# Performance work log

Hardware: AMD Instinct MI355X
Metric: run time of the kernel (lower is better)

Reference implementation:

```python
import jax, jax.numpy as jnp
import numpy as np

MAX_NEUMANN_STEPS = 8

def _neumann_inverse(A):
    # (I + A)^{-1} for strictly lower-triangular A via Neumann series with repeated squaring.
    T = A.shape[-1]
    I = jnp.eye(T, dtype=A.dtype)
    neg_A = -A
    B_power = neg_A
    N = I + neg_A
    for _ in range(MAX_NEUMANN_STEPS - 1):
        B_power = jnp.matmul(B_power, B_power)
        N = N + jnp.matmul(B_power, N)
    return N

def setup_inputs() -> dict:
    key = jax.random.key(0)
    ks = jax.random.split(key, 6)
    B, H, T, Dk, Dv = 16, 32, 256, 128, 128
    q = jax.random.normal(ks[0], (B, H, T, Dk), dtype=jnp.float32)
    k = jax.random.normal(ks[1], (B, H, T, Dk), dtype=jnp.float32)
    k = k / jnp.linalg.norm(k, axis=-1, keepdims=True)  # keys are L2-normalized
    v = jax.random.normal(ks[2], (B, H, T, Dv), dtype=jnp.float32)
    # log-space decay gate: small negative values so exp(g) in (0,1)
    g = -0.05 * jax.random.uniform(ks[3], (B, H, T), dtype=jnp.float32)
    beta = jax.random.uniform(ks[4], (B, H, T), dtype=jnp.float32)
    S0 = jax.random.normal(ks[5], (B, H, Dk, Dv), dtype=jnp.float32)
    return {"q": q, "k": k, "v": v, "g": g, "beta": beta, "last_recurrent_state": S0}

def reference(q, k, v, g, beta, last_recurrent_state):
    S = last_recurrent_state                               # (B,H,Dk,Dv)
    g_cumsum = jnp.cumsum(g, axis=-1)                      # (B,H,T)
    KKT = jnp.matmul(k, k.swapaxes(-1, -2))                # (B,H,T,T)
    g_diff = g_cumsum[..., :, None] - g_cumsum[..., None, :]
    A_full = beta[..., None] * jnp.exp(g_diff) * KKT
    A = jnp.tril(A_full, k=-1)                             # strictly lower triangular
    T_inv = _neumann_inverse(A)                            # (I+A)^{-1}
    beta_g = (beta * jnp.exp(g_cumsum))[..., None]         # (B,H,T,1)
    W = jnp.matmul(T_inv, beta_g * k)                      # (B,H,T,Dk)
    U = jnp.matmul(T_inv, beta[..., None] * v)             # (B,H,T,Dv)
    v_new = U - jnp.matmul(W, S)                           # (B,H,T,Dv)
    inter = jnp.matmul(q, S) * jnp.exp(g_cumsum)[..., None]
    QKT = jnp.matmul(q, k.swapaxes(-1, -2))
    causal = jnp.tril(jnp.exp(g_diff), k=0)
    intra = jnp.matmul(causal * QKT, v_new)
    output = inter + intra                                 # (B,H,T,Dv)
    g_last = g_cumsum[..., -1:]                            # (B,H,1)
    S_new = S * jnp.exp(g_last)[..., None]
    g_scale = jnp.exp(g_last[..., None] - g_cumsum[..., None])  # (B,H,T,1)
    S_new = S_new + jnp.matmul(k.swapaxes(-2, -1), v_new * g_scale)
    return jnp.concatenate([output.reshape(-1), S_new.reshape(-1)], axis=0)
```

## Files before the change

### kernel.cpp

```cpp
#include <hip/hip_runtime.h>
#include <hip/hip_bf16.h>

typedef __attribute__((ext_vector_type(8))) short short8;
typedef __attribute__((ext_vector_type(4))) short short4v;
typedef __attribute__((ext_vector_type(4))) float f32x4;

#define DEVI static __device__ __forceinline__

constexpr int T_SEQ = 256, DK = 128, DV = 128, CH = 64, NCH = 4;
constexpr int NPAIR = 16 * 32;
constexpr size_t OUT_ELEMS = (size_t)NPAIR * T_SEQ * DV;

constexpr int OFF_SB   = 0;
constexpr int OFF_KC   = 32768;
constexpr int OFF_KCT  = 49152;
constexpr int OFF_KRQS = 65536;
constexpr int OFF_V    = 81920;
constexpr int OFF_B    = 98304;
constexpr int OFF_BT   = 106496;
constexpr int OFF_NT   = 114688;
constexpr int OFF_GC   = 122880;
constexpr int OFF_BETA = 123904;
constexpr int OFF_EPOS = 124928;
constexpr int OFF_ENEG = 125184;
constexpr int OFF_WS   = 125440;
constexpr int LDS_BYTES = 125472;

DEVI unsigned short f2bf(float f) {
  union { float f; unsigned u; } a; a.f = f;
  unsigned r = a.u + 0x7fffu + ((a.u >> 16) & 1u);
  return (unsigned short)(r >> 16);
}
DEVI float bf2f(unsigned short h) {
  union { unsigned u; float f; } a; a.u = ((unsigned)h) << 16;
  return a.f;
}

DEVI f32x4 mfma(short8 a, short8 b, f32x4 c) {
  return __builtin_amdgcn_mfma_f32_16x16x32_bf16(a, b, c, 0, 0, 0);
}

DEVI short8 ldf(const char* s, int stride, int row, int k0) {
  return *(const short8*)(s + row * stride + ((((row & 7) << 4)) ^ (k0 * 2)));
}
DEVI void st4(char* s, int stride, int row, int col0, f32x4 v) {
  short4v p;
  p[0] = (short)f2bf(v[0]); p[1] = (short)f2bf(v[1]);
  p[2] = (short)f2bf(v[2]); p[3] = (short)f2bf(v[3]);
  *(short4v*)(s + row * stride + (((row & 7) << 4) ^ (col0 * 2))) = p;
}
DEVI void st1(char* s, int stride, int row, int col, float f) {
  *(unsigned short*)(s + row * stride + (((row & 7) << 4) ^ (col * 2))) = f2bf(f);
}

__global__ __launch_bounds__(512, 1)
void cra_fwd(const float* __restrict__ qg_, const float* __restrict__ kg_,
             const float* __restrict__ vg_, const float* __restrict__ gg_,
             const float* __restrict__ bg_, const float* __restrict__ s0g_,
             float* __restrict__ outg_)
{
  extern __shared__ char sm[];
  const int tid = threadIdx.x;
  const int lane = tid & 63, w = tid >> 6;
  const int l15 = lane & 15, l4 = lane >> 4;
  const int pair = blockIdx.x;

  const size_t rowbase = (size_t)pair * T_SEQ;
  const float* qg = qg_ + rowbase * DK;
  const float* kg = kg_ + rowbase * DK;
  const float* vg = vg_ + rowbase * DV;
  float* outg = outg_ + rowbase * DV;
  float* soutg = outg_ + OUT_ELEMS + (size_t)pair * DK * DV;

  float* gc    = (float*)(sm + OFF_GC);
  float* bet   = (float*)(sm + OFF_BETA);
  float* eposA = (float*)(sm + OFF_EPOS);
  float* enegA = (float*)(sm + OFF_ENEG);
  float* wsum  = (float*)(sm + OFF_WS);

  f32x4 Sacc[8];
  {
    const float* Sp = s0g_ + (size_t)pair * DK * DV;
    const int dk0 = w * 16 + l4 * 4;
#pragma unroll
    for (int tn = 0; tn < 8; ++tn) {
      const int dv = tn * 16 + l15;
#pragma unroll
      for (int rr = 0; rr < 4; ++rr)
        Sacc[tn][rr] = Sp[(size_t)(dk0 + rr) * DV + dv];
    }
  }

  if (tid < 256) {
    float x = gg_[rowbase + tid];
    bet[tid] = bg_[rowbase + tid];
#pragma unroll
    for (int d = 1; d < 64; d <<= 1) {
      float y = __shfl_up(x, d, 64);
      if (lane >= d) x += y;
    }
    if (lane == 63) wsum[w] = x;
    gc[tid] = x;
  }
  __syncthreads();
  if (tid < 256) {
    float pre = 0.f;
    for (int j = 0; j < w; ++j) pre += wsum[j];
    gc[tid] += pre;
  }
  __syncthreads();

  const int r = tid >> 3, u = tid & 7;
  const f32x4 zero = {0.f, 0.f, 0.f, 0.f};
  const int tmB = (w >> 1) * 16;

#pragma unroll 1
  for (int c = 0; c < NCH; ++c) {
    const int t0 = c * CH;
    if (tid < 64) {
      const float base = (c == 0) ? 0.f : gc[t0 - 1];
      const float lc = gc[t0 + tid] - base;
      eposA[tid] = __expf(lc);
      enegA[tid] = __expf(-lc);
    }
    const float4* kp = (const float4*)(kg + (size_t)(t0 + r) * DK);
    const float4* vp = (const float4*)(vg + (size_t)(t0 + r) * DV);
    float4 kv[4], vv[4];
#pragma unroll
    for (int j = 0; j < 4; ++j) { kv[j] = kp[u + 8 * j]; vv[j] = vp[u + 8 * j]; }
    __syncthreads();

    {
      const float be = bet[t0 + r], ep = eposA[r], en = enegA[r];
      const float krs = be * ep;
#pragma unroll
      for (int j = 0; j < 4; ++j) {
        const int col0 = 4 * (u + 8 * j);
        const float kf[4] = {kv[j].x, kv[j].y, kv[j].z, kv[j].w};
        const float vf[4] = {vv[j].x, vv[j].y, vv[j].z, vv[j].w};
        short4v pr, pc;
#pragma unroll
        for (int e = 0; e < 4; ++e) {
          pr[e] = (short)f2bf(kf[e] * krs);
          pc[e] = (short)f2bf(kf[e] * en);
        }
        *(short4v*)(sm + OFF_KRQS + r * 256 + (((r & 7) << 4) ^ (col0 * 2))) = pr;
        *(short4v*)(sm + OFF_KC   + r * 256 + (((r & 7) << 4) ^ (col0 * 2))) = pc;
#pragma unroll
        for (int e = 0; e < 4; ++e) {
          const int d = col0 + e;
          *(unsigned short*)(sm + OFF_KCT + d * 128 + (((d & 7) << 4) ^ (r * 2))) = f2bf(kf[e] * en);
          *(unsigned short*)(sm + OFF_V   + d * 128 + (((d & 7) << 4) ^ (r * 2))) = f2bf(vf[e] * be);
        }
      }
      const int dk0 = w * 16 + l4 * 4;
#pragma unroll
      for (int tn = 0; tn < 8; ++tn)
        st4(sm + OFF_SB, 256, tn * 16 + l15, dk0, Sacc[tn]);
    }
    __syncthreads();

    f32x4 nreg[2];
#pragma unroll
    for (int s = 0; s < 2; ++s) {
      const int tn = (w & 1) * 2 + s;
      f32x4 acc = zero;
#pragma unroll
      for (int ks = 0; ks < 4; ++ks) {
        short8 af = ldf(sm + OFF_KRQS, 256, tmB + l15,   ks * 32 + l4 * 8);
        short8 bf = ldf(sm + OFF_KC,   256, tn * 16 + l15, ks * 32 + l4 * 8);
        acc = mfma(af, bf, acc);
      }
      const int i0 = tmB + l4 * 4, jj = tn * 16 + l15;
      f32x4 nr;
#pragma unroll
      for (int rr = 0; rr < 4; ++rr) {
        const int i = i0 + rr;
        const float Bv = (i > jj) ? -acc[rr] : 0.f;
        st1(sm + OFF_B,  128, i, jj, Bv);
        st1(sm + OFF_BT, 128, jj, i, Bv);
        nr[rr] = ((i == jj) ? 1.f : 0.f) + Bv;
      }
      nreg[s] = nr;
      st4(sm + OFF_NT, 128, jj, i0, nr);
    }

#pragma unroll
    for (int s = 0; s < 4; ++s) {
      const int tn = (w & 1) * 4 + s;
      f32x4 acc = zero;
#pragma unroll
      for (int ks = 0; ks < 4; ++ks) {
        short8 af = ldf(sm + OFF_KRQS, 256, tmB + l15,   ks * 32 + l4 * 8);
        short8 bf = ldf(sm + OFF_SB,   256, tn * 16 + l15, ks * 32 + l4 * 8);
        acc = mfma(af, bf, acc);
      }
      const int dv = tn * 16 + l15, i0 = tmB + l4 * 4;
      char* p = sm + OFF_V + dv * 128 + (((dv & 7) << 4) ^ (i0 * 2));
      short4v old = *(const short4v*)p;
      short4v nw;
#pragma unroll
      for (int rr = 0; rr < 4; ++rr)
        nw[rr] = (short)f2bf(bf2f((unsigned short)old[rr]) - acc[rr]);
      *(short4v*)p = nw;
    }
    const float4* qp = (const float4*)(qg + (size_t)(t0 + r) * DK);
    float4 qv[4];
#pragma unroll
    for (int j = 0; j < 4; ++j) qv[j] = qp[u + 8 * j];
    __syncthreads();

#pragma unroll
    for (int it = 0; it < 5; ++it) {
      f32x4 b2[2];
#pragma unroll
      for (int s = 0; s < 2; ++s) {
        const int tn = (w & 1) * 2 + s;
        f32x4 acc = zero;
#pragma unroll
        for (int ks = 0; ks < 2; ++ks) {
          short8 af = ldf(sm + OFF_B,  128, tmB + l15,   ks * 32 + l4 * 8);
          short8 bf = ldf(sm + OFF_BT, 128, tn * 16 + l15, ks * 32 + l4 * 8);
          acc = mfma(af, bf, acc);
        }
        b2[s] = acc;
      }
      __syncthreads();
#pragma unroll
      for (int s = 0; s < 2; ++s) {
        const int tn = (w & 1) * 2 + s;
        const int i0 = tmB + l4 * 4, jj = tn * 16 + l15;
#pragma unroll
        for (int rr = 0; rr < 4; ++rr) st1(sm + OFF_B, 128, i0 + rr, jj, b2[s][rr]);
        if (it < 4) st4(sm + OFF_BT, 128, jj, i0, b2[s]);
      }
      __syncthreads();
#pragma unroll
      for (int s = 0; s < 2; ++s) {
        const int tn = (w & 1) * 2 + s;
#pragma unroll
        for (int ks = 0; ks < 2; ++ks) {
          short8 af = ldf(sm + OFF_B,  128, tmB + l15,   ks * 32 + l4 * 8);
          short8 bf = ldf(sm + OFF_NT, 128, tn * 16 + l15, ks * 32 + l4 * 8);
          nreg[s] = mfma(af, bf, nreg[s]);
        }
      }
      __syncthreads();
#pragma unroll
      for (int s = 0; s < 2; ++s) {
        const int tn = (w & 1) * 2 + s;
        const int i0 = tmB + l4 * 4, jj = tn * 16 + l15;
        st4(sm + OFF_NT, 128, jj, i0, nreg[s]);
        if (it == 4) {
#pragma unroll
          for (int rr = 0; rr < 4; ++rr) st1(sm + OFF_BT, 128, i0 + rr, jj, nreg[s][rr]);
        }
      }
      __syncthreads();
    }

    f32x4 vn[4];
#pragma unroll
    for (int s = 0; s < 4; ++s) {
      const int tn = (w & 1) * 4 + s;
      f32x4 acc = zero;
#pragma unroll
      for (int ks = 0; ks < 2; ++ks) {
        short8 af = ldf(sm + OFF_BT, 128, tmB + l15,   ks * 32 + l4 * 8);
        short8 bf = ldf(sm + OFF_V,  128, tn * 16 + l15, ks * 32 + l4 * 8);
        acc = mfma(af, bf, acc);
      }
      vn[s] = acc;
    }
    __syncthreads();
#pragma unroll
    for (int s = 0; s < 4; ++s) {
      const int tn = (w & 1) * 4 + s;
      st4(sm + OFF_V, 128, tn * 16 + l15, tmB + l4 * 4, vn[s]);
    }
    {
      const float ep = eposA[r];
#pragma unroll
      for (int j = 0; j < 4; ++j) {
        const int col0 = 4 * (u + 8 * j);
        const float qf[4] = {qv[j].x, qv[j].y, qv[j].z, qv[j].w};
        short4v pq;
#pragma unroll
        for (int e = 0; e < 4; ++e) pq[e] = (short)f2bf(qf[e] * ep);
        *(short4v*)(sm + OFF_KRQS + r * 256 + (((r & 7) << 4) ^ (col0 * 2))) = pq;
      }
    }
    __syncthreads();

    f32x4 outA[4];
#pragma unroll
    for (int s = 0; s < 4; ++s) {
      const int tn = (w & 1) * 4 + s;
      f32x4 acc = zero;
#pragma unroll
      for (int ks = 0; ks < 4; ++ks) {
        short8 af = ldf(sm + OFF_KRQS, 256, tmB + l15,   ks * 32 + l4 * 8);
        short8 bf = ldf(sm + OFF_SB,   256, tn * 16 + l15, ks * 32 + l4 * 8);
        acc = mfma(af, bf, acc);
      }
      outA[s] = acc;
    }
#pragma unroll
    for (int s = 0; s < 2; ++s) {
      const int tn = (w & 1) * 2 + s;
      f32x4 acc = zero;
#pragma unroll
      for (int ks = 0; ks < 4; ++ks) {
        short8 af = ldf(sm + OFF_KRQS, 256, tmB + l15,   ks * 32 + l4 * 8);
        short8 bf = ldf(sm + OFF_KC,   256, tn * 16 + l15, ks * 32 + l4 * 8);
        acc = mfma(af, bf, acc);
      }
      const int i0 = tmB + l4 * 4, jj = tn * 16 + l15;
#pragma unroll
      for (int rr = 0; rr < 4; ++rr)
        st1(sm + OFF_B, 128, i0 + rr, jj, (jj <= i0 + rr) ? acc[rr] : 0.f);
    }
    __syncthreads();
#pragma unroll
    for (int s = 0; s < 4; ++s) {
      const int tn = (w & 1) * 4 + s;
#pragma unroll
      for (int ks = 0; ks < 2; ++ks) {
        short8 af = ldf(sm + OFF_B, 128, tmB + l15,   ks * 32 + l4 * 8);
        short8 bf = ldf(sm + OFF_V, 128, tn * 16 + l15, ks * 32 + l4 * 8);
        outA[s] = mfma(af, bf, outA[s]);
      }
    }
    {
      const float eG = eposA[CH - 1];
#pragma unroll
      for (int tn = 0; tn < 8; ++tn) {
#pragma unroll
        for (int ks = 0; ks < 2; ++ks) {
          short8 af = ldf(sm + OFF_KCT, 128, w * 16 + l15,  ks * 32 + l4 * 8);
          short8 bf = ldf(sm + OFF_V,   128, tn * 16 + l15, ks * 32 + l4 * 8);
          Sacc[tn] = mfma(af, bf, Sacc[tn]);
        }
#pragma unroll
        for (int rr = 0; rr < 4; ++rr) Sacc[tn][rr] *= eG;
      }
    }
    __syncthreads();
    {
      float* OST = (float*)(sm + OFF_KC);
#pragma unroll
      for (int s = 0; s < 4; ++s) {
        const int tn = (w & 1) * 4 + s;
        const int i0 = tmB + l4 * 4, dv = tn * 16 + l15;
#pragma unroll
        for (int rr = 0; rr < 4; ++rr) OST[(i0 + rr) * 128 + dv] = outA[s][rr];
      }
    }
    __syncthreads();
    {
      float4* og = (float4*)(outg + (size_t)t0 * DV);
      const float4* os = (const float4*)(sm + OFF_KC);
#pragma unroll
      for (int j = 0; j < 4; ++j) og[tid + 512 * j] = os[tid + 512 * j];
    }
    __syncthreads();
  }

  {
    float* SST = (float*)sm;
    const int dk0 = w * 16 + l4 * 4;
#pragma unroll
    for (int tn = 0; tn < 8; ++tn) {
      const int dv = tn * 16 + l15;
#pragma unroll
      for (int rr = 0; rr < 4; ++rr) SST[(dk0 + rr) * 128 + dv] = Sacc[tn][rr];
    }
  }
  __syncthreads();
  {
    float4* sg = (float4*)soutg;
    const float4* ss = (const float4*)sm;
#pragma unroll
    for (int j = 0; j < 8; ++j) sg[tid + 512 * j] = ss[tid + 512 * j];
  }
}

extern "C" void kernel_launch(void* const* d_in, const int* in_sizes, int n_in,
                              void* d_out, int out_size, void* d_ws, size_t ws_size,
                              hipStream_t stream) {
  (void)in_sizes; (void)n_in; (void)out_size; (void)d_ws; (void)ws_size;
  const float* q  = (const float*)d_in[0];
  const float* k  = (const float*)d_in[1];
  const float* v  = (const float*)d_in[2];
  const float* g  = (const float*)d_in[3];
  const float* b  = (const float*)d_in[4];
  const float* s0 = (const float*)d_in[5];
  hipFuncSetAttribute((const void*)cra_fwd,
                      hipFuncAttributeMaxDynamicSharedMemorySize, LDS_BYTES);
  hipLaunchKernelGGL(cra_fwd, dim3(NPAIR), dim3(512), LDS_BYTES, stream,
                     q, k, v, g, b, s0, (float*)d_out);
}
```

Baseline: 305.3 us.

## Apply Neumann inverse directly to value block via ping-pong power matrices

Instead of building the explicit inverse matrix N by repeated squaring and then multiplying it into V, the loop now updates the transformed value block X in place (X += P·X) while squaring the power matrix, with ping-pong P/PT buffers. Fewer barriers per iteration are needed. LDS swizzles widen to 16-row patterns, next-chunk k/v loads are prefetched into registers, and output and final state are written straight to global memory instead of being staged through LDS. This raises LDS use and makes the final global stores less coalesced. The bf16 rounding of X on every iteration may also change accuracy.

Result: slower. 391.0 us (+28.1%).

```diff
diff --git a/kernel.cpp b/kernel.cpp
--- a/kernel.cpp
+++ b/kernel.cpp
@@ -8,23 +8,24 @@
 #define DEVI static __device__ __forceinline__
 
 constexpr int T_SEQ = 256, DK = 128, DV = 128, CH = 64, NCH = 4;
-constexpr int NPAIR = 16 * 32;
+constexpr int NPAIR = 512;
 constexpr size_t OUT_ELEMS = (size_t)NPAIR * T_SEQ * DV;
 
 constexpr int OFF_SB   = 0;
 constexpr int OFF_KC   = 32768;
-constexpr int OFF_KCT  = 49152;
-constexpr int OFF_KRQS = 65536;
-constexpr int OFF_V    = 81920;
-constexpr int OFF_B    = 98304;
-constexpr int OFF_BT   = 106496;
-constexpr int OFF_NT   = 114688;
-constexpr int OFF_GC   = 122880;
-constexpr int OFF_BETA = 123904;
-constexpr int OFF_EPOS = 124928;
-constexpr int OFF_ENEG = 125184;
-constexpr int OFF_WS   = 125440;
-constexpr int LDS_BYTES = 125472;
+constexpr int OFF_KRQS = 49152;
+constexpr int OFF_XT   = 65536;
+constexpr int OFF_KCT  = 98304;
+constexpr int OFF_PA   = 114688;
+constexpr int OFF_PTA  = 124928;
+constexpr int OFF_PB   = 135168;
+constexpr int OFF_PTB  = 145408;
+constexpr int OFF_EPOS = 155648;
+constexpr int OFF_ENEG = 155904;
+constexpr int OFF_GC   = 156160;
+constexpr int OFF_BETA = 157184;
+constexpr int OFF_WS   = 158208;
+constexpr int LDS_BYTES = 158240;
 
 DEVI unsigned short f2bf(float f) {
   union { float f; unsigned u; } a; a.f = f;
@@ -35,22 +36,26 @@
   union { unsigned u; float f; } a; a.u = ((unsigned)h) << 16;
   return a.f;
 }
-
 DEVI f32x4 mfma(short8 a, short8 b, f32x4 c) {
   return __builtin_amdgcn_mfma_f32_16x16x32_bf16(a, b, c, 0, 0, 0);
 }
-
-DEVI short8 ldf(const char* s, int stride, int row, int k0) {
-  return *(const short8*)(s + row * stride + ((((row & 7) << 4)) ^ (k0 * 2)));
-}
-DEVI void st4(char* s, int stride, int row, int col0, f32x4 v) {
+DEVI short8 ld16(const char* s, int row, int kb) {
+  return *(const short8*)(s + row * 256 + (((row & 15) << 4) ^ kb));
+}
+DEVI void st4_16(char* s, int row, int col0, short4v p) {
+  *(short4v*)(s + row * 256 + (((row & 15) << 4) ^ (col0 * 2))) = p;
+}
+DEVI short8 ld8(const char* s, int stride, int row, int kb) {
+  return *(const short8*)(s + row * stride + (((row & 7) << 4) ^ kb));
+}
+DEVI void st4_8(char* s, int stride, int row, int col0, short4v p) {
+  *(short4v*)(s + row * stride + (((row & 7) << 4) ^ (col0 * 2))) = p;
+}
+DEVI short4v pack4(f32x4 v) {
   short4v p;
   p[0] = (short)f2bf(v[0]); p[1] = (short)f2bf(v[1]);
   p[2] = (short)f2bf(v[2]); p[3] = (short)f2bf(v[3]);
-  *(short4v*)(s + row * stride + (((row & 7) << 4) ^ (col0 * 2))) = p;
-}
-DEVI void st1(char* s, int stride, int row, int col, float f) {
-  *(unsigned short*)(s + row * stride + (((row & 7) << 4) ^ (col * 2))) = f2bf(f);
+  return p;
 }
 
 __global__ __launch_bounds__(512, 1)
@@ -63,6 +68,7 @@
   const int tid = threadIdx.x;
   const int lane = tid & 63, w = tid >> 6;
   const int l15 = lane & 15, l4 = lane >> 4;
+  const int kb0 = l4 * 16;
   const int pair = blockIdx.x;
 
   const size_t rowbase = (size_t)pair * T_SEQ;
@@ -91,6 +97,14 @@
     }
   }
 
+  const int r = tid >> 3, u = tid & 7;
+  float4 kv[4], vv[4];
+  {
+    const float4* kp = (const float4*)(kg + (size_t)r * DK);
+    const float4* vp = (const float4*)(vg + (size_t)r * DV);
+#pragma unroll
+    for (int j = 0; j < 4; ++j) { kv[j] = kp[u + 8 * j]; vv[j] = vp[u + 8 * j]; }
+  }
   if (tid < 256) {
     float x = gg_[rowbase + tid];
     bet[tid] = bg_[rowbase + tid];
@@ -110,7 +124,6 @@
   }
   __syncthreads();
 
-  const int r = tid >> 3, u = tid & 7;
   const f32x4 zero = {0.f, 0.f, 0.f, 0.f};
   const int tmB = (w >> 1) * 16;
 
@@ -123,11 +136,6 @@
       eposA[tid] = __expf(lc);
       enegA[tid] = __expf(-lc);
     }
-    const float4* kp = (const float4*)(kg + (size_t)(t0 + r) * DK);
-    const float4* vp = (const float4*)(vg + (size_t)(t0 + r) * DV);
-    float4 kv[4], vv[4];
-#pragma unroll
-    for (int j = 0; j < 4; ++j) { kv[j] = kp[u + 8 * j]; vv[j] = vp[u + 8 * j]; }
     __syncthreads();
 
     {
@@ -144,244 +152,212 @@
           pr[e] = (short)f2bf(kf[e] * krs);
           pc[e] = (short)f2bf(kf[e] * en);
         }
-        *(short4v*)(sm + OFF_KRQS + r * 256 + (((r & 7) << 4) ^ (col0 * 2))) = pr;
-        *(short4v*)(sm + OFF_KC   + r * 256 + (((r & 7) << 4) ^ (col0 * 2))) = pc;
+        st4_16(sm + OFF_KRQS, r, col0, pr);
+        st4_16(sm + OFF_KC,   r, col0, pc);
 #pragma unroll
         for (int e = 0; e < 4; ++e) {
           const int d = col0 + e;
           *(unsigned short*)(sm + OFF_KCT + d * 128 + (((d & 7) << 4) ^ (r * 2))) = f2bf(kf[e] * en);
-          *(unsigned short*)(sm + OFF_V   + d * 128 + (((d & 7) << 4) ^ (r * 2))) = f2bf(vf[e] * be);
+          *(unsigned short*)(sm + OFF_XT  + d * 256 + (((d & 15) << 4) ^ (r * 2))) = f2bf(vf[e] * be);
         }
       }
       const int dk0 = w * 16 + l4 * 4;
 #pragma unroll
       for (int tn = 0; tn < 8; ++tn)
-        st4(sm + OFF_SB, 256, tn * 16 + l15, dk0, Sacc[tn]);
+        st4_16(sm + OFF_SB, tn * 16 + l15, dk0, pack4(Sacc[tn]));
     }
     __syncthreads();
 
-    f32x4 nreg[2];
+    float4 qv[4];
+    {
+      const float4* qp = (const float4*)(qg + (size_t)(t0 + r) * DK);
+#pragma unroll
+      for (int j = 0; j < 4; ++j) qv[j] = qp[u + 8 * j];
+    }
 #pragma unroll
     for (int s = 0; s < 2; ++s) {
-      const int tn = (w & 1) * 2 + s;
-      f32x4 acc = zero;
-#pragma unroll
-      for (int ks = 0; ks < 4; ++ks) {
-        short8 af = ldf(sm + OFF_KRQS, 256, tmB + l15,   ks * 32 + l4 * 8);
-        short8 bf = ldf(sm + OFF_KC,   256, tn * 16 + l15, ks * 32 + l4 * 8);
-        acc = mfma(af, bf, acc);
-      }
-      const int i0 = tmB + l4 * 4, jj = tn * 16 + l15;
-      f32x4 nr;
+      const int nt = (w & 1) * 2 + s;
+      f32x4 acc = zero;
+#pragma unroll
+      for (int ks = 0; ks < 4; ++ks)
+        acc = mfma(ld16(sm + OFF_KRQS, tmB + l15, ks * 64 + kb0),
+                   ld16(sm + OFF_KC,   nt * 16 + l15, ks * 64 + kb0), acc);
+      const int jj = nt * 16 + l15, i0 = tmB + l4 * 4;
+      short4v p;
 #pragma unroll
       for (int rr = 0; rr < 4; ++rr) {
         const int i = i0 + rr;
-        const float Bv = (i > jj) ? -acc[rr] : 0.f;
-        st1(sm + OFF_B,  128, i, jj, Bv);
-        st1(sm + OFF_BT, 128, jj, i, Bv);
-        nr[rr] = ((i == jj) ? 1.f : 0.f) + Bv;
-      }
-      nreg[s] = nr;
-      st4(sm + OFF_NT, 128, jj, i0, nr);
-    }
-
+        p[rr] = (short)f2bf((i > jj) ? -acc[rr] : 0.f);
+      }
+      st4_8(sm + OFF_PTA, 160, jj, i0, p);
+    }
+#pragma unroll
+    for (int s = 0; s < 2; ++s) {
+      const int nt = (w & 1) * 2 + s;
+      f32x4 acc = zero;
+#pragma unroll
+      for (int ks = 0; ks < 4; ++ks)
+        acc = mfma(ld16(sm + OFF_KC,   tmB + l15, ks * 64 + kb0),
+                   ld16(sm + OFF_KRQS, nt * 16 + l15, ks * 64 + kb0), acc);
+      const int ii = nt * 16 + l15, j0 = tmB + l4 * 4;
+      short4v p;
+#pragma unroll
+      for (int rr = 0; rr < 4; ++rr) {
+        const int j = j0 + rr;
+        p[rr] = (short)f2bf((ii > j) ? -acc[rr] : 0.f);
+      }
+      st4_8(sm + OFF_PA, 160, ii, j0, p);
+    }
 #pragma unroll
     for (int s = 0; s < 4; ++s) {
-      const int tn = (w & 1) * 4 + s;
-      f32x4 acc = zero;
-#pragma unroll
-      for (int ks = 0; ks < 4; ++ks) {
-        short8 af = ldf(sm + OFF_KRQS, 256, tmB + l15,   ks * 32 + l4 * 8);
-        short8 bf = ldf(sm + OFF_SB,   256, tn * 16 + l15, ks * 32 + l4 * 8);
-        acc = mfma(af, bf, acc);
-      }
-      const int dv = tn * 16 + l15, i0 = tmB + l4 * 4;
-      char* p = sm + OFF_V + dv * 128 + (((dv & 7) << 4) ^ (i0 * 2));
-      short4v old = *(const short4v*)p;
-      short4v nw;
+      const int dvt = (w & 1) * 4 + s;
+      f32x4 acc = zero;
+#pragma unroll
+      for (int ks = 0; ks < 4; ++ks)
+        acc = mfma(ld16(sm + OFF_KRQS, tmB + l15, ks * 64 + kb0),
+                   ld16(sm + OFF_SB,   dvt * 16 + l15, ks * 64 + kb0), acc);
+      const int dv = dvt * 16 + l15, i0 = tmB + l4 * 4;
+      char* p = sm + OFF_XT + dv * 256 + (((dv & 15) << 4) ^ (i0 * 2));
+      short4v old = *(const short4v*)p, nw;
 #pragma unroll
       for (int rr = 0; rr < 4; ++rr)
         nw[rr] = (short)f2bf(bf2f((unsigned short)old[rr]) - acc[rr]);
       *(short4v*)p = nw;
     }
-    const float4* qp = (const float4*)(qg + (size_t)(t0 + r) * DK);
-    float4 qv[4];
-#pragma unroll
-    for (int j = 0; j < 4; ++j) qv[j] = qp[u + 8 * j];
+
+#pragma unroll
+    for (int it = 0; it < 6; ++it) {
+      __syncthreads();
+      const char* Pc  = (it & 1) ? sm + OFF_PB  : sm + OFF_PA;
+      const char* PTc = (it & 1) ? sm + OFF_PTB : sm + OFF_PTA;
+      char* Pn  = (it & 1) ? sm + OFF_PA  : sm + OFF_PB;
+      char* PTn = (it & 1) ? sm + OFF_PTA : sm + OFF_PTB;
+
+      short8 bb[2];
+#pragma unroll
+      for (int ks = 0; ks < 2; ++ks)
+        bb[ks] = ld16(sm + OFF_XT, w * 16 + l15, ks * 64 + kb0);
+      f32x4 xa[4];
+#pragma unroll
+      for (int itile = 0; itile < 4; ++itile) {
+        f32x4 acc = zero;
+#pragma unroll
+        for (int ks = 0; ks < 2; ++ks)
+          acc = mfma(ld8(Pc, 160, itile * 16 + l15, ks * 64 + kb0), bb[ks], acc);
+        xa[itile] = acc;
+      }
+      if (it == 0) {
+        const float ep = eposA[r];
+#pragma unroll
+        for (int j = 0; j < 4; ++j) {
+          const int col0 = 4 * (u + 8 * j);
+          const float qf[4] = {qv[j].x, qv[j].y, qv[j].z, qv[j].w};
+          short4v pq;
+#pragma unroll
+          for (int e = 0; e < 4; ++e) pq[e] = (short)f2bf(qf[e] * ep);
+          st4_16(sm + OFF_KRQS, r, col0, pq);
+        }
+      }
+      if (it < 5) {
+#pragma unroll
+        for (int s = 0; s < 2; ++s) {
+          const int nt = (w & 1) * 2 + s;
+          f32x4 a1 = zero, a2 = zero;
+#pragma unroll
+          for (int ks = 0; ks < 2; ++ks) {
+            a1 = mfma(ld8(Pc,  160, tmB + l15, ks * 64 + kb0),
+                      ld8(PTc, 160, nt * 16 + l15, ks * 64 + kb0), a1);
+            a2 = mfma(ld8(PTc, 160, tmB + l15, ks * 64 + kb0),
+                      ld8(Pc,  160, nt * 16 + l15, ks * 64 + kb0), a2);
+          }
+          st4_8(PTn, 160, nt * 16 + l15, tmB + l4 * 4, pack4(a1));
+          st4_8(Pn,  160, nt * 16 + l15, tmB + l4 * 4, pack4(a2));
+        }
+      }
+#pragma unroll
+      for (int itile = 0; itile < 4; ++itile) {
+        const int row = w * 16 + l15;
+        char* p = sm + OFF_XT + row * 256 + (((row & 15) << 4) ^ ((itile * 16 + l4 * 4) * 2));
+        short4v old = *(const short4v*)p, nw;
+#pragma unroll
+        for (int rr = 0; rr < 4; ++rr)
+          nw[rr] = (short)f2bf(bf2f((unsigned short)old[rr]) + xa[itile][rr]);
+        *(short4v*)p = nw;
+      }
+    }
     __syncthreads();
 
-#pragma unroll
-    for (int it = 0; it < 5; ++it) {
-      f32x4 b2[2];
-#pragma unroll
-      for (int s = 0; s < 2; ++s) {
-        const int tn = (w & 1) * 2 + s;
-        f32x4 acc = zero;
-#pragma unroll
-        for (int ks = 0; ks < 2; ++ks) {
-          short8 af = ldf(sm + OFF_B,  128, tmB + l15,   ks * 32 + l4 * 8);
-          short8 bf = ldf(sm + OFF_BT, 128, tn * 16 + l15, ks * 32 + l4 * 8);
-          acc = mfma(af, bf, acc);
-        }
-        b2[s] = acc;
-      }
-      __syncthreads();
-#pragma unroll
-      for (int s = 0; s < 2; ++s) {
-        const int tn = (w & 1) * 2 + s;
-        const int i0 = tmB + l4 * 4, jj = tn * 16 + l15;
-#pragma unroll
-        for (int rr = 0; rr < 4; ++rr) st1(sm + OFF_B, 128, i0 + rr, jj, b2[s][rr]);
-        if (it < 4) st4(sm + OFF_BT, 128, jj, i0, b2[s]);
-      }
-      __syncthreads();
-#pragma unroll
-      for (int s = 0; s < 2; ++s) {
-        const int tn = (w & 1) * 2 + s;
-#pragma unroll
-        for (int ks = 0; ks < 2; ++ks) {
-          short8 af = ldf(sm + OFF_B,  128, tmB + l15,   ks * 32 + l4 * 8);
-          short8 bf = ldf(sm + OFF_NT, 128, tn * 16 + l15, ks * 32 + l4 * 8);
-          nreg[s] = mfma(af, bf, nreg[s]);
-        }
-      }
-      __syncthreads();
-#pragma unroll
-      for (int s = 0; s < 2; ++s) {
-        const int tn = (w & 1) * 2 + s;
-        const int i0 = tmB + l4 * 4, jj = tn * 16 + l15;
-        st4(sm + OFF_NT, 128, jj, i0, nreg[s]);
-        if (it == 4) {
-#pragma unroll
-          for (int rr = 0; rr < 4; ++rr) st1(sm + OFF_BT, 128, i0 + rr, jj, nreg[s][rr]);
-        }
-      }
-      __syncthreads();
-    }
-
-    f32x4 vn[4];
+    f32x4 outA[4];
 #pragma unroll
     for (int s = 0; s < 4; ++s) {
-      const int tn = (w & 1) * 4 + s;
-      f32x4 acc = zero;
-#pragma unroll
-      for (int ks = 0; ks < 2; ++ks) {
-        short8 af = ldf(sm + OFF_BT, 128, tmB + l15,   ks * 32 + l4 * 8);
-        short8 bf = ldf(sm + OFF_V,  128, tn * 16 + l15, ks * 32 + l4 * 8);
-        acc = mfma(af, bf, acc);
-      }
-      vn[s] = acc;
-    }
-    __syncthreads();
-#pragma unroll
-    for (int s = 0; s < 4; ++s) {
-      const int tn = (w & 1) * 4 + s;
-      st4(sm + OFF_V, 128, tn * 16 + l15, tmB + l4 * 4, vn[s]);
-    }
-    {
-      const float ep = eposA[r];
-#pragma unroll
-      for (int j = 0; j < 4; ++j) {
-        const int col0 = 4 * (u + 8 * j);
-        const float qf[4] = {qv[j].x, qv[j].y, qv[j].z, qv[j].w};
-        short4v pq;
-#pragma unroll
-        for (int e = 0; e < 4; ++e) pq[e] = (short)f2bf(qf[e] * ep);
-        *(short4v*)(sm + OFF_KRQS + r * 256 + (((r & 7) << 4) ^ (col0 * 2))) = pq;
-      }
-    }
-    __syncthreads();
-
-    f32x4 outA[4];
-#pragma unroll
-    for (int s = 0; s < 4; ++s) {
-      const int tn = (w & 1) * 4 + s;
-      f32x4 acc = zero;
-#pragma unroll
-      for (int ks = 0; ks < 4; ++ks) {
-        short8 af = ldf(sm + OFF_KRQS, 256, tmB + l15,   ks * 32 + l4 * 8);
-        short8 bf = ldf(sm + OFF_SB,   256, tn * 16 + l15, ks * 32 + l4 * 8);
-        acc = mfma(af, bf, acc);
-      }
+      const int dvt = (w & 1) * 4 + s;
+      f32x4 acc = zero;
+#pragma unroll
+      for (int ks = 0; ks < 4; ++ks)
+        acc = mfma(ld16(sm + OFF_KRQS, tmB + l15, ks * 64 + kb0),
+                   ld16(sm + OFF_SB,   dvt * 16 + l15, ks * 64 + kb0), acc);
       outA[s] = acc;
     }
 #pragma unroll
     for (int s = 0; s < 2; ++s) {
-      const int tn = (w & 1) * 2 + s;
-      f32x4 acc = zero;
-#pragma unroll
-      for (int ks = 0; ks < 4; ++ks) {
-        short8 af = ldf(sm + OFF_KRQS, 256, tmB + l15,   ks * 32 + l4 * 8);
-        short8 bf = ldf(sm + OFF_KC,   256, tn * 16 + l15, ks * 32 + l4 * 8);
-        acc = mfma(af, bf, acc);
-      }
-      const int i0 = tmB + l4 * 4, jj = tn * 16 + l15;
-#pragma unroll
-      for (int rr = 0; rr < 4; ++rr)
-        st1(sm + OFF_B, 128, i0 + rr, jj, (jj <= i0 + rr) ? acc[rr] : 0.f);
-    }
-    __syncthreads();
-#pragma unroll
-    for (int s = 0; s < 4; ++s) {
-      const int tn = (w & 1) * 4 + s;
-#pragma unroll
-      for (int ks = 0; ks < 2; ++ks) {
-        short8 af = ldf(sm + OFF_B, 128, tmB + l15,   ks * 32 + l4 * 8);
-        short8 bf = ldf(sm + OFF_V, 128, tn * 16 + l15, ks * 32 + l4 * 8);
-        outA[s] = mfma(af, bf, outA[s]);
-      }
+      const int nt = (w & 1) * 2 + s;
+      f32x4 acc = zero;
+#pragma unroll
+      for (int ks = 0; ks < 4; ++ks)
+        acc = mfma(ld16(sm + OFF_KC,   tmB + l15, ks * 64 + kb0),
+                   ld16(sm + OFF_KRQS, nt * 16 + l15, ks * 64 + kb0), acc);
+      const int ii = nt * 16 + l15, j0 = tmB + l4 * 4;
+      short4v p;
+#pragma unroll
+      for (int rr = 0; rr < 4; ++rr) {
+        const int j = j0 + rr;
+        p[rr] = (short)f2bf((ii >= j) ? acc[rr] : 0.f);
+      }
+      st4_8(sm + OFF_PA, 160, ii, j0, p);
     }
     {
       const float eG = eposA[CH - 1];
 #pragma unroll
       for (int tn = 0; tn < 8; ++tn) {
 #pragma unroll
-        for (int ks = 0; ks < 2; ++ks) {
-          short8 af = ldf(sm + OFF_KCT, 128, w * 16 + l15,  ks * 32 + l4 * 8);
-          short8 bf = ldf(sm + OFF_V,   128, tn * 16 + l15, ks * 32 + l4 * 8);
-          Sacc[tn] = mfma(af, bf, Sacc[tn]);
-        }
+        for (int ks = 0; ks < 2; ++ks)
+          Sacc[tn] = mfma(ld8(sm + OFF_KCT, 128, w * 16 + l15, ks * 64 + kb0),
+                          ld16(sm + OFF_XT, tn * 16 + l15, ks * 64 + kb0), Sacc[tn]);
 #pragma unroll
         for (int rr = 0; rr < 4; ++rr) Sacc[tn][rr] *= eG;
       }
     }
     __syncthreads();
-    {
-      float* OST = (float*)(sm + OFF_KC);
-#pragma unroll
-      for (int s = 0; s < 4; ++s) {
-        const int tn = (w & 1) * 4 + s;
-        const int i0 = tmB + l4 * 4, dv = tn * 16 + l15;
-#pragma unroll
-        for (int rr = 0; rr < 4; ++rr) OST[(i0 + rr) * 128 + dv] = outA[s][rr];
-      }
-    }
-    __syncthreads();
-    {
-      float4* og = (float4*)(outg + (size_t)t0 * DV);
-      const float4* os = (const float4*)(sm + OFF_KC);
-#pragma unroll
-      for (int j = 0; j < 4; ++j) og[tid + 512 * j] = os[tid + 512 * j];
-    }
-    __syncthreads();
+
+    if (c + 1 < NCH) {
+      const float4* kp = (const float4*)(kg + (size_t)((c + 1) * CH + r) * DK);
+      const float4* vp = (const float4*)(vg + (size_t)((c + 1) * CH + r) * DV);
+#pragma unroll
+      for (int j = 0; j < 4; ++j) { kv[j] = kp[u + 8 * j]; vv[j] = vp[u + 8 * j]; }
+    }
+#pragma unroll
+    for (int s = 0; s < 4; ++s) {
+      const int dvt = (w & 1) * 4 + s;
+#pragma unroll
+      for (int ks = 0; ks < 2; ++ks)
+        outA[s] = mfma(ld8(sm + OFF_PA, 160, tmB + l15, ks * 64 + kb0),
+                       ld16(sm + OFF_XT, dvt * 16 + l15, ks * 64 + kb0), outA[s]);
+      const int dv = dvt * 16 + l15, i0 = tmB + l4 * 4;
+#pragma unroll
+      for (int rr = 0; rr < 4; ++rr)
+        outg[(size_t)(t0 + i0 + rr) * DV + dv] = outA[s][rr];
+    }
   }
 
   {
-    float* SST = (float*)sm;
     const int dk0 = w * 16 + l4 * 4;
 #pragma unroll
     for (int tn = 0; tn < 8; ++tn) {
       const int dv = tn * 16 + l15;
 #pragma unroll
-      for (int rr = 0; rr < 4; ++rr) SST[(dk0 + rr) * 128 + dv] = Sacc[tn][rr];
-    }
-  }
-  __syncthreads();
-  {
-    float4* sg = (float4*)soutg;
-    const float4* ss = (const float4*)sm;
-#pragma unroll
-    for (int j = 0; j < 8; ++j) sg[tid + 512 * j] = ss[tid + 512 * j];
+      for (int rr = 0; rr < 4; ++rr)
+        soutg[(size_t)(dk0 + rr) * DV + dv] = Sacc[tn][rr];
+    }
   }
 }
 
```
